# Optimization experiments

Hardware: AMD Instinct MI355X
Metric: run time of the kernel (lower is better)

## Reference

```python
import jax, jax.numpy as jnp
import numpy as np

B, H, S, D = 2, 8, 2048, 64
TEMPERATURE = 8.0  # sqrt(D)
NEG = -1.0e9


def setup_inputs() -> dict:
    key = jax.random.key(0)
    kq, kk, kv, km = jax.random.split(key, 4)
    q = jax.random.normal(kq, (B, H, S, D), dtype=jnp.float32)
    k = jax.random.normal(kk, (B, H, S, D), dtype=jnp.float32)
    v = jax.random.normal(kv, (B, H, S, D), dtype=jnp.float32)
    mask = jax.random.randint(km, (B, 1, 1, S), 0, 2, dtype=jnp.int32)
    return {"q": q, "k": k, "v": v, "mask": mask}


def reference(q, k, v, mask):
    # scores: [B,H,S,S]
    att = jnp.einsum('bhqd,bhkd->bhqk', q / TEMPERATURE, k)
    att = jnp.where(mask == 0, NEG, att)
    att = jax.nn.softmax(att, axis=-1)
    return jnp.einsum('bhqk,bhkd->bhqd', att, v)
```

## Files before the change

kernel.cpp:

```cpp
#include <hip/hip_runtime.h>
#include <hip/hip_bf16.h>

#define SDIM 2048
#define DDIM 64
#define HNUM 8
#define QBLK 64
#define KVBLK 64
#define NTHR 256
#define NT (SDIM / KVBLK)
#define NSPLIT 2
#define LDP 72
#define NEGV -1.0e9f
#define LOG2E 1.44269504088896f
#define FIXMAX 12.0f

#define WS_KH 0u
#define WS_VH 4194304u
#define WS_O1 8388608u
#define WS_ML 12582912u
#define WS_IDX 13107200u
#define WS_CNT 13123584u

typedef __bf16 bf16x8 __attribute__((ext_vector_type(8)));
typedef __bf16 bf16x4 __attribute__((ext_vector_type(4)));
typedef float f32x4 __attribute__((ext_vector_type(4)));
typedef unsigned short u16;
typedef u16 u16x4 __attribute__((ext_vector_type(4)));
typedef u16 u16x8 __attribute__((ext_vector_type(8)));

__device__ __forceinline__ u16 f2bf(float f) {
    unsigned u = __float_as_uint(f);
    u += 0x7FFFu + ((u >> 16) & 1u);
    return (u16)(u >> 16);
}
__device__ __forceinline__ float bf2f(u16 h) {
    return __uint_as_float((unsigned)h << 16);
}

union U8 { u16 u[8]; u16x8 v; bf16x8 b; };

#define GLD16(g, l) __builtin_amdgcn_global_load_lds( \
    (const __attribute__((address_space(1))) unsigned int*)(g), \
    (__attribute__((address_space(3))) unsigned int*)(l), 16, 0, 0)

__global__ __launch_bounds__(NTHR)
void attn_scan(const int* __restrict__ MK, char* __restrict__ ws) {
    const int b = blockIdx.x, t = threadIdx.x;
    const int ln = t & 63, wv = t >> 6;
    const int* m = MK + (size_t)b * SDIM;
    int* idx = (int*)(ws + WS_IDX) + b * SDIM;

    int vals[8], cnt = 0;
    #pragma unroll
    for (int e = 0; e < 8; ++e) {
        vals[e] = m[t * 8 + e];
        cnt += (vals[e] != 0);
    }
    int inc = cnt;
    #pragma unroll
    for (int off = 1; off < 64; off <<= 1) {
        int n = __shfl_up(inc, off);
        if (ln >= off) inc += n;
    }
    __shared__ int wtot[4];
    if (ln == 63) wtot[wv] = inc;
    __syncthreads();
    int wbase = 0;
    #pragma unroll
    for (int w = 0; w < 4; ++w) if (w < wv) wbase += wtot[w];
    const int total = wtot[0] + wtot[1] + wtot[2] + wtot[3];
    int pos = wbase + inc - cnt;
    #pragma unroll
    for (int e = 0; e < 8; ++e)
        if (vals[e]) idx[pos++] = t * 8 + e;
    if (t == 0) ((int*)(ws + WS_CNT))[b] = total;
    #pragma unroll
    for (int e = 0; e < 8; ++e) {
        const int j = t * 8 + e;
        if (j >= total) idx[j] = 0;
    }
}

__global__ __launch_bounds__(NTHR)
void attn_prep(const float* __restrict__ K, const float* __restrict__ V,
               char* __restrict__ ws) {
    __shared__ float sT[64][68];
    const int t = threadIdx.x;
    const int kt = blockIdx.x, bh = blockIdx.y;
    const int kv0 = kt * KVBLK;
    const int cnt = ((const int*)(ws + WS_CNT))[bh >> 3];
    if (kv0 >= ((cnt + KVBLK - 1) & ~(KVBLK - 1))) return;
    const size_t base = (size_t)bh * SDIM * DDIM;
    const int r = t >> 2, c16 = (t & 3) * 16;
    const int sw = (r & 7) << 4;
    const int orig = ((const int*)(ws + WS_IDX))[(bh >> 3) * SDIM + kv0 + r];

    {
        const float* kp = K + base + (size_t)orig * DDIM + c16;
        char* khrow = ws + WS_KH + ((size_t)bh * SDIM + kv0 + r) * 128;
        #pragma unroll
        for (int j = 0; j < 2; ++j) {
            const float4 a = *(const float4*)(kp + 8 * j);
            const float4 c = *(const float4*)(kp + 8 * j + 4);
            float f[8] = {a.x, a.y, a.z, a.w, c.x, c.y, c.z, c.w};
            U8 h;
            #pragma unroll
            for (int e = 0; e < 8; ++e) h.u[e] = f2bf(f[e]);
            *(u16x8*)(khrow + ((2 * c16 + 16 * j) ^ sw)) = h.v;
        }
    }
    {
        const float* vp = V + base + (size_t)orig * DDIM + c16;
        #pragma unroll
        for (int j = 0; j < 4; ++j)
            *(float4*)&sT[r][c16 + 4 * j] = *(const float4*)(vp + 4 * j);
    }
    __syncthreads();
    {
        char* vhrow = ws + WS_VH + ((size_t)(bh * NT + kt) * 64 + r) * 128;
        #pragma unroll
        for (int j2 = 0; j2 < 2; ++j2) {
            U8 h;
            #pragma unroll
            for (int e = 0; e < 8; ++e)
                h.u[e] = f2bf(sT[c16 + 8 * j2 + e][r]);
            *(u16x8*)(vhrow + ((2 * c16 + 16 * j2) ^ sw)) = h.v;
        }
    }
}

__global__ __launch_bounds__(NTHR, 4)
void attn_main(const float* __restrict__ Q, char* __restrict__ ws,
               float* __restrict__ O) {
    __shared__ __align__(16) u16 sK[2][KVBLK * DDIM];
    __shared__ __align__(16) u16 sV[DDIM * KVBLK];
    __shared__ __align__(16) u16 sP[QBLK][LDP];

    const int tid = threadIdx.x;
    const int wv = tid >> 6, ln = tid & 63;
    const int g = ln >> 4, mi = ln & 15;
    const int bh = blockIdx.y, b = bh >> 3;
    const int split = blockIdx.z;
    const size_t base = (size_t)bh * SDIM * DDIM;
    const int qrow = blockIdx.x * QBLK + 16 * wv + mi;

    const int L = ((const int*)(ws + WS_CNT))[b];
    const int nt = (L + KVBLK - 1) >> 6;
    const int half = (nt + 1) >> 1;
    const int t0 = split ? half : 0;
    const int tn = split ? nt : half;

    const int sw = (mi & 7) << 4;
    const int c0 = (16 * g) ^ sw;
    const int c1 = (64 + 16 * g) ^ sw;

    bf16x8 qhi[2], qlo[2];
    {
        const float* qp = Q + base + (size_t)qrow * DDIM;
        #pragma unroll
        for (int ks = 0; ks < 2; ++ks) {
            const float4 a = *(const float4*)(qp + 32 * ks + 8 * g);
            const float4 c = *(const float4*)(qp + 32 * ks + 8 * g + 4);
            float f[8] = {a.x, a.y, a.z, a.w, c.x, c.y, c.z, c.w};
            U8 h, l;
            #pragma unroll
            for (int e = 0; e < 8; ++e) {
                float fs = f[e] * (0.125f * LOG2E);
                u16 hh = f2bf(fs);
                h.u[e] = hh;
                l.u[e] = f2bf(fs - bf2f(hh));
            }
            qhi[ks] = h.b;
            qlo[ks] = l.b;
        }
    }

    const char* kgl = ws + WS_KH + (size_t)bh * SDIM * 128;
    const char* vgl = ws + WS_VH + (size_t)bh * NT * 8192;
    const int chunk = wv * 2;

    f32x4 zero4 = {0.f, 0.f, 0.f, 0.f};
    f32x4 oacc[4];
    #pragma unroll
    for (int i = 0; i < 4; ++i) oacc[i] = zero4;
    float lrun = 0.f;

    if (t0 < tn) {
        {
            const char* src = kgl + (size_t)t0 * 8192;
            #pragma unroll
            for (int p = 0; p < 2; ++p) {
                const int off = (chunk + p) * 1024;
                GLD16(src + off + ln * 16, (char*)&sK[0][0] + off);
            }
        }

        int cur = 0;
        for (int kt = t0; kt < tn; ++kt) {
            {
                const char* src = vgl + (size_t)kt * 8192;
                #pragma unroll
                for (int p = 0; p < 2; ++p) {
                    const int off = (chunk + p) * 1024;
                    GLD16(src + off + ln * 16, (char*)&sV[0] + off);
                }
            }
            {
                const int kn = (kt + 1 < tn) ? kt + 1 : t0;
                const char* src = kgl + (size_t)kn * 8192;
                char* dst = (char*)&sK[cur ^ 1][0];
                #pragma unroll
                for (int p = 0; p < 2; ++p) {
                    const int off = (chunk + p) * 1024;
                    GLD16(src + off + ln * 16, dst + off);
                }
            }
            asm volatile("s_waitcnt vmcnt(4)" ::: "memory");
            __builtin_amdgcn_s_barrier();

            const char* kb = (const char*)&sK[cur][0] + mi * 128;
            float s[4][4];
            #pragma unroll
            for (int mt = 0; mt < 4; ++mt) {
                f32x4 acc = zero4;
                const bf16x8 ah0 = *(const bf16x8*)(kb + mt * 2048 + c0);
                const bf16x8 ah1 = *(const bf16x8*)(kb + mt * 2048 + c1);
                acc = __builtin_amdgcn_mfma_f32_16x16x32_bf16(ah0, qhi[0], acc, 0, 0, 0);
                acc = __builtin_amdgcn_mfma_f32_16x16x32_bf16(ah0, qlo[0], acc, 0, 0, 0);
                acc = __builtin_amdgcn_mfma_f32_16x16x32_bf16(ah1, qhi[1], acc, 0, 0, 0);
                acc = __builtin_amdgcn_mfma_f32_16x16x32_bf16(ah1, qlo[1], acc, 0, 0, 0);
                s[mt][0] = acc[0]; s[mt][1] = acc[1];
                s[mt][2] = acc[2]; s[mt][3] = acc[3];
            }
            const int rem = L - kt * KVBLK;
            if (rem < KVBLK) {
                #pragma unroll
                for (int mt = 0; mt < 4; ++mt)
                    #pragma unroll
                    for (int r = 0; r < 4; ++r)
                        if (16 * mt + 4 * g + r >= rem) s[mt][r] = NEGV;
            }

            #pragma unroll
            for (int mt = 0; mt < 4; ++mt) {
                bf16x4 pw;
                #pragma unroll
                for (int r = 0; r < 4; ++r) {
                    const float p = __builtin_amdgcn_exp2f(s[mt][r] - FIXMAX);
                    pw[r] = (__bf16)p;
                    lrun += p;
                }
                *(bf16x4*)&sP[16 * wv + mi][16 * mt + 4 * g] = pw;
            }

            asm volatile("s_waitcnt vmcnt(2)" ::: "memory");
            __builtin_amdgcn_s_barrier();

            const char* vb = (const char*)&sV[0] + mi * 128;
            const bf16x8 pf0 = *(const bf16x8*)&sP[16 * wv + mi][8 * g];
            const bf16x8 pf1 = *(const bf16x8*)&sP[16 * wv + mi][32 + 8 * g];
            #pragma unroll
            for (int mt = 0; mt < 4; ++mt) {
                const bf16x8 vh0 = *(const bf16x8*)(vb + mt * 2048 + c0);
                const bf16x8 vh1 = *(const bf16x8*)(vb + mt * 2048 + c1);
                oacc[mt] = __builtin_amdgcn_mfma_f32_16x16x32_bf16(vh0, pf0, oacc[mt], 0, 0, 0);
                oacc[mt] = __builtin_amdgcn_mfma_f32_16x16x32_bf16(vh1, pf1, oacc[mt], 0, 0, 0);
            }
            __builtin_amdgcn_s_barrier();
            cur ^= 1;
        }
    }

    lrun += __shfl_xor(lrun, 16);
    lrun += __shfl_xor(lrun, 32);
    const float inv = lrun > 0.f ? 1.0f / lrun : 0.f;
    if (split == 0) {
        float* op = O + base + (size_t)qrow * DDIM;
        #pragma unroll
        for (int mt = 0; mt < 4; ++mt) {
            float4 o;
            o.x = oacc[mt][0] * inv;
            o.y = oacc[mt][1] * inv;
            o.z = oacc[mt][2] * inv;
            o.w = oacc[mt][3] * inv;
            *(float4*)(op + 16 * mt + 4 * g) = o;
        }
    } else {
        u16* op1 = (u16*)(ws + WS_O1) + ((size_t)bh * SDIM + qrow) * DDIM;
        #pragma unroll
        for (int mt = 0; mt < 4; ++mt) {
            u16x4 o;
            #pragma unroll
            for (int r = 0; r < 4; ++r) o[r] = f2bf(oacc[mt][r] * inv);
            *(u16x4*)(op1 + 16 * mt + 4 * g) = o;
        }
    }
    if (g == 0) {
        float* lp = (float*)(ws + WS_ML) + ((size_t)(split * 2 * HNUM + bh) * SDIM + qrow);
        *lp = lrun;
    }
}

__global__ __launch_bounds__(NTHR)
void attn_combine(const char* __restrict__ ws, float* __restrict__ O) {
    const int t = threadIdx.x;
    const size_t grow = (size_t)blockIdx.x * 16 + (t >> 4);
    const int e4 = (t & 15) * 4;
    const float* ml = (const float*)(ws + WS_ML);
    float w0 = ml[grow];
    float w1 = ml[(size_t)2 * HNUM * SDIM + grow];
    const float swt = w0 + w1;
    const float inv = swt > 0.f ? 1.0f / swt : 0.f;
    w0 *= inv; w1 *= inv;
    float* op = O + grow * DDIM + e4;
    const float4 o0 = *(const float4*)op;
    const u16x4 o1 = *(const u16x4*)((const u16*)(ws + WS_O1) + grow * DDIM + e4);
    float4 r;
    r.x = o0.x * w0 + bf2f(o1[0]) * w1;
    r.y = o0.y * w0 + bf2f(o1[1]) * w1;
    r.z = o0.z * w0 + bf2f(o1[2]) * w1;
    r.w = o0.w * w0 + bf2f(o1[3]) * w1;
    *(float4*)op = r;
}

extern "C" void kernel_launch(void* const* d_in, const int* in_sizes, int n_in,
                              void* d_out, int out_size, void* d_ws, size_t ws_size,
                              hipStream_t stream) {
    const float* q  = (const float*)d_in[0];
    const float* k  = (const float*)d_in[1];
    const float* v  = (const float*)d_in[2];
    const int*   mk = (const int*)d_in[3];
    float* o = (float*)d_out;
    char* ws = (char*)d_ws;

    attn_scan<<<2, NTHR, 0, stream>>>(mk, ws);

    dim3 pgrid(NT, 2 * HNUM);
    attn_prep<<<pgrid, NTHR, 0, stream>>>(k, v, ws);

    dim3 grid(SDIM / QBLK, 2 * HNUM, NSPLIT);
    attn_main<<<grid, NTHR, 0, stream>>>(q, ws, o);

    dim3 cgrid((2 * HNUM * SDIM) / 16);
    attn_combine<<<cgrid, NTHR, 0, stream>>>(ws, o);
}
```

Baseline: 41.14 us.

## Split KV across waves with register-held P and cross-wave LDS reduction

Restructures attn_main so each wave handles a 16-key quarter of every KV tile for all 64 query rows, instead of 16 query rows against all keys. P stays in registers and feeds a 16x16x16 bf16 MFMA directly, which removes the sP LDS round trip and the per-tile barriers. The V pre-pack layout changes to suit that. Q is now a single bf16 term instead of the hi/lo split, halving QK MFMAs at some accuracy cost. The partial outputs are summed through LDS at the end. This adds a final reduction and raises register pressure (launch bound 3).

```diff
diff --git a/kernel.cpp b/kernel.cpp
--- a/kernel.cpp
+++ b/kernel.cpp
@@ -9,7 +9,6 @@
 #define NTHR 256
 #define NT (SDIM / KVBLK)
 #define NSPLIT 2
-#define LDP 72
 #define NEGV -1.0e9f
 #define LOG2E 1.44269504088896f
 #define FIXMAX 12.0f
@@ -23,6 +22,7 @@
 
 typedef __bf16 bf16x8 __attribute__((ext_vector_type(8)));
 typedef __bf16 bf16x4 __attribute__((ext_vector_type(4)));
+typedef short s16x4 __attribute__((ext_vector_type(4)));
 typedef float f32x4 __attribute__((ext_vector_type(4)));
 typedef unsigned short u16;
 typedef u16 u16x4 __attribute__((ext_vector_type(4)));
@@ -42,6 +42,15 @@
 #define GLD16(g, l) __builtin_amdgcn_global_load_lds( \
     (const __attribute__((address_space(1))) unsigned int*)(g), \
     (__attribute__((address_space(3))) unsigned int*)(l), 16, 0, 0)
+
+__device__ __forceinline__ f32x4 mfma16(s16x4 a, s16x4 b, f32x4 c) {
+#if __has_builtin(__builtin_amdgcn_mfma_f32_16x16x16bf16_1k)
+    return __builtin_amdgcn_mfma_f32_16x16x16bf16_1k(a, b, c, 0, 0, 0);
+#else
+    asm("v_mfma_f32_16x16x16_bf16 %0, %1, %2, %0" : "+v"(c) : "v"(a), "v"(b));
+    return c;
+#endif
+}
 
 __global__ __launch_bounds__(NTHR)
 void attn_scan(const int* __restrict__ MK, char* __restrict__ ws) {
@@ -117,24 +126,26 @@
     }
     __syncthreads();
     {
-        char* vhrow = ws + WS_VH + ((size_t)(bh * NT + kt) * 64 + r) * 128;
-        #pragma unroll
-        for (int j2 = 0; j2 < 2; ++j2) {
-            U8 h;
-            #pragma unroll
-            for (int e = 0; e < 8; ++e)
-                h.u[e] = f2bf(sT[c16 + 8 * j2 + e][r]);
-            *(u16x8*)(vhrow + ((2 * c16 + 16 * j2) ^ sw)) = h.v;
-        }
-    }
-}
-
-__global__ __launch_bounds__(NTHR, 4)
+        const int kvq = t >> 6, d = t & 63;
+        char* dst = ws + WS_VH + ((size_t)(bh * NT + kt)) * 8192 + kvq * 2048 + d * 32;
+        #pragma unroll
+        for (int gk = 0; gk < 4; ++gk) {
+            u16x4 h;
+            #pragma unroll
+            for (int e = 0; e < 4; ++e)
+                h[e] = f2bf(sT[kvq * 16 + 4 * gk + e][d]);
+            *(u16x4*)(dst + (((gk ^ ((d >> 2) & 3)) << 3))) = h;
+        }
+    }
+}
+
+__global__ __launch_bounds__(NTHR, 3)
 void attn_main(const float* __restrict__ Q, char* __restrict__ ws,
                float* __restrict__ O) {
-    __shared__ __align__(16) u16 sK[2][KVBLK * DDIM];
-    __shared__ __align__(16) u16 sV[DDIM * KVBLK];
-    __shared__ __align__(16) u16 sP[QBLK][LDP];
+    __shared__ __align__(16) union LdsU {
+        struct { u16 k[2][4096]; u16 v[2][4096]; } st;
+        struct { float o[3][64][64]; float l[4][64]; } red;
+    } lds;
 
     const int tid = threadIdx.x;
     const int wv = tid >> 6, ln = tid & 63;
@@ -142,7 +153,7 @@
     const int bh = blockIdx.y, b = bh >> 3;
     const int split = blockIdx.z;
     const size_t base = (size_t)bh * SDIM * DDIM;
-    const int qrow = blockIdx.x * QBLK + 16 * wv + mi;
+    const int q0 = blockIdx.x * QBLK;
 
     const int L = ((const int*)(ws + WS_CNT))[b];
     const int nt = (L + KVBLK - 1) >> 6;
@@ -153,152 +164,152 @@
     const int sw = (mi & 7) << 4;
     const int c0 = (16 * g) ^ sw;
     const int c1 = (64 + 16 * g) ^ sw;
-
-    bf16x8 qhi[2], qlo[2];
-    {
-        const float* qp = Q + base + (size_t)qrow * DDIM;
+    const int vslot = (g ^ (mi >> 2)) << 3;
+
+    bf16x8 qf[4][2];
+    #pragma unroll
+    for (int qt = 0; qt < 4; ++qt) {
+        const float* qp = Q + base + (size_t)(q0 + qt * 16 + mi) * DDIM;
         #pragma unroll
         for (int ks = 0; ks < 2; ++ks) {
             const float4 a = *(const float4*)(qp + 32 * ks + 8 * g);
             const float4 c = *(const float4*)(qp + 32 * ks + 8 * g + 4);
             float f[8] = {a.x, a.y, a.z, a.w, c.x, c.y, c.z, c.w};
-            U8 h, l;
-            #pragma unroll
-            for (int e = 0; e < 8; ++e) {
-                float fs = f[e] * (0.125f * LOG2E);
-                u16 hh = f2bf(fs);
-                h.u[e] = hh;
-                l.u[e] = f2bf(fs - bf2f(hh));
-            }
-            qhi[ks] = h.b;
-            qlo[ks] = l.b;
-        }
-    }
-
-    const char* kgl = ws + WS_KH + (size_t)bh * SDIM * 128;
-    const char* vgl = ws + WS_VH + (size_t)bh * NT * 8192;
-    const int chunk = wv * 2;
+            U8 h;
+            #pragma unroll
+            for (int e = 0; e < 8; ++e) h.u[e] = f2bf(f[e] * (0.125f * LOG2E));
+            qf[qt][ks] = h.b;
+        }
+    }
+
+    const char* kq_src = ws + WS_KH + (size_t)bh * SDIM * 128;
+    const char* vq_src = ws + WS_VH + (size_t)bh * NT * 8192;
+    char* sKbase = (char*)lds.st.k;
+    char* sVbase = (char*)lds.st.v;
 
     f32x4 zero4 = {0.f, 0.f, 0.f, 0.f};
-    f32x4 oacc[4];
-    #pragma unroll
-    for (int i = 0; i < 4; ++i) oacc[i] = zero4;
-    float lrun = 0.f;
+    f32x4 oacc[4][4];
+    #pragma unroll
+    for (int i = 0; i < 4; ++i)
+        #pragma unroll
+        for (int j = 0; j < 4; ++j) oacc[i][j] = zero4;
+    float lrun[4] = {0.f, 0.f, 0.f, 0.f};
+
+#define STAGE_QTR(kt_, buf_) do { \
+    const char* ksrc_ = kq_src + (size_t)(kt_) * 8192 + wv * 2048; \
+    char* kdst_ = sKbase + (buf_) * 8192 + wv * 2048; \
+    GLD16(ksrc_ + ln * 16, kdst_); \
+    GLD16(ksrc_ + 1024 + ln * 16, kdst_ + 1024); \
+    const char* vsrc_ = vq_src + (size_t)(kt_) * 8192 + wv * 2048; \
+    char* vdst_ = sVbase + (buf_) * 8192 + wv * 2048; \
+    GLD16(vsrc_ + ln * 16, vdst_); \
+    GLD16(vsrc_ + 1024 + ln * 16, vdst_ + 1024); \
+} while (0)
 
     if (t0 < tn) {
-        {
-            const char* src = kgl + (size_t)t0 * 8192;
-            #pragma unroll
-            for (int p = 0; p < 2; ++p) {
-                const int off = (chunk + p) * 1024;
-                GLD16(src + off + ln * 16, (char*)&sK[0][0] + off);
-            }
-        }
-
+        STAGE_QTR(t0, 0);
         int cur = 0;
         for (int kt = t0; kt < tn; ++kt) {
-            {
-                const char* src = vgl + (size_t)kt * 8192;
+            const int kn = (kt + 1 < tn) ? kt + 1 : t0;
+            STAGE_QTR(kn, cur ^ 1);
+            asm volatile("s_waitcnt vmcnt(4)" ::: "memory");
+
+            const char* kb = sKbase + cur * 8192 + wv * 2048 + mi * 128;
+            const bf16x8 a0 = *(const bf16x8*)(kb + c0);
+            const bf16x8 a1 = *(const bf16x8*)(kb + c1);
+            f32x4 s[4];
+            #pragma unroll
+            for (int qt = 0; qt < 4; ++qt) {
+                f32x4 acc = zero4;
+                acc = __builtin_amdgcn_mfma_f32_16x16x32_bf16(a0, qf[qt][0], acc, 0, 0, 0);
+                acc = __builtin_amdgcn_mfma_f32_16x16x32_bf16(a1, qf[qt][1], acc, 0, 0, 0);
+                s[qt] = acc;
+            }
+            const int kbase = kt * KVBLK + wv * 16;
+            if (kbase + 16 > L) {
                 #pragma unroll
-                for (int p = 0; p < 2; ++p) {
-                    const int off = (chunk + p) * 1024;
-                    GLD16(src + off + ln * 16, (char*)&sV[0] + off);
-                }
-            }
-            {
-                const int kn = (kt + 1 < tn) ? kt + 1 : t0;
-                const char* src = kgl + (size_t)kn * 8192;
-                char* dst = (char*)&sK[cur ^ 1][0];
-                #pragma unroll
-                for (int p = 0; p < 2; ++p) {
-                    const int off = (chunk + p) * 1024;
-                    GLD16(src + off + ln * 16, dst + off);
-                }
-            }
-            asm volatile("s_waitcnt vmcnt(4)" ::: "memory");
-            __builtin_amdgcn_s_barrier();
-
-            const char* kb = (const char*)&sK[cur][0] + mi * 128;
-            float s[4][4];
-            #pragma unroll
-            for (int mt = 0; mt < 4; ++mt) {
-                f32x4 acc = zero4;
-                const bf16x8 ah0 = *(const bf16x8*)(kb + mt * 2048 + c0);
-                const bf16x8 ah1 = *(const bf16x8*)(kb + mt * 2048 + c1);
-                acc = __builtin_amdgcn_mfma_f32_16x16x32_bf16(ah0, qhi[0], acc, 0, 0, 0);
-                acc = __builtin_amdgcn_mfma_f32_16x16x32_bf16(ah0, qlo[0], acc, 0, 0, 0);
-                acc = __builtin_amdgcn_mfma_f32_16x16x32_bf16(ah1, qhi[1], acc, 0, 0, 0);
-                acc = __builtin_amdgcn_mfma_f32_16x16x32_bf16(ah1, qlo[1], acc, 0, 0, 0);
-                s[mt][0] = acc[0]; s[mt][1] = acc[1];
-                s[mt][2] = acc[2]; s[mt][3] = acc[3];
-            }
-            const int rem = L - kt * KVBLK;
-            if (rem < KVBLK) {
-                #pragma unroll
-                for (int mt = 0; mt < 4; ++mt)
+                for (int qt = 0; qt < 4; ++qt)
                     #pragma unroll
                     for (int r = 0; r < 4; ++r)
-                        if (16 * mt + 4 * g + r >= rem) s[mt][r] = NEGV;
-            }
-
-            #pragma unroll
-            for (int mt = 0; mt < 4; ++mt) {
-                bf16x4 pw;
+                        if (kbase + 4 * g + r >= L) s[qt][r] = NEGV;
+            }
+
+            bf16x4 pw[4];
+            #pragma unroll
+            for (int qt = 0; qt < 4; ++qt) {
                 #pragma unroll
                 for (int r = 0; r < 4; ++r) {
-                    const float p = __builtin_amdgcn_exp2f(s[mt][r] - FIXMAX);
-                    pw[r] = (__bf16)p;
-                    lrun += p;
+                    const float p = __builtin_amdgcn_exp2f(s[qt][r] - FIXMAX);
+                    pw[qt][r] = (__bf16)p;
+                    lrun[qt] += p;
                 }
-                *(bf16x4*)&sP[16 * wv + mi][16 * mt + 4 * g] = pw;
-            }
-
-            asm volatile("s_waitcnt vmcnt(2)" ::: "memory");
-            __builtin_amdgcn_s_barrier();
-
-            const char* vb = (const char*)&sV[0] + mi * 128;
-            const bf16x8 pf0 = *(const bf16x8*)&sP[16 * wv + mi][8 * g];
-            const bf16x8 pf1 = *(const bf16x8*)&sP[16 * wv + mi][32 + 8 * g];
-            #pragma unroll
-            for (int mt = 0; mt < 4; ++mt) {
-                const bf16x8 vh0 = *(const bf16x8*)(vb + mt * 2048 + c0);
-                const bf16x8 vh1 = *(const bf16x8*)(vb + mt * 2048 + c1);
-                oacc[mt] = __builtin_amdgcn_mfma_f32_16x16x32_bf16(vh0, pf0, oacc[mt], 0, 0, 0);
-                oacc[mt] = __builtin_amdgcn_mfma_f32_16x16x32_bf16(vh1, pf1, oacc[mt], 0, 0, 0);
-            }
-            __builtin_amdgcn_s_barrier();
+            }
+
+            const char* vb = sVbase + cur * 8192 + wv * 2048 + mi * 32 + vslot;
+            #pragma unroll
+            for (int dt = 0; dt < 4; ++dt) {
+                const s16x4 vf = *(const s16x4*)(vb + dt * 512);
+                #pragma unroll
+                for (int qt = 0; qt < 4; ++qt)
+                    oacc[qt][dt] = mfma16(vf, __builtin_bit_cast(s16x4, pw[qt]), oacc[qt][dt]);
+            }
             cur ^= 1;
         }
     }
 
-    lrun += __shfl_xor(lrun, 16);
-    lrun += __shfl_xor(lrun, 32);
-    const float inv = lrun > 0.f ? 1.0f / lrun : 0.f;
-    if (split == 0) {
-        float* op = O + base + (size_t)qrow * DDIM;
-        #pragma unroll
-        for (int mt = 0; mt < 4; ++mt) {
-            float4 o;
-            o.x = oacc[mt][0] * inv;
-            o.y = oacc[mt][1] * inv;
-            o.z = oacc[mt][2] * inv;
-            o.w = oacc[mt][3] * inv;
-            *(float4*)(op + 16 * mt + 4 * g) = o;
-        }
-    } else {
-        u16* op1 = (u16*)(ws + WS_O1) + ((size_t)bh * SDIM + qrow) * DDIM;
-        #pragma unroll
-        for (int mt = 0; mt < 4; ++mt) {
-            u16x4 o;
-            #pragma unroll
-            for (int r = 0; r < 4; ++r) o[r] = f2bf(oacc[mt][r] * inv);
-            *(u16x4*)(op1 + 16 * mt + 4 * g) = o;
-        }
+    #pragma unroll
+    for (int qt = 0; qt < 4; ++qt) {
+        lrun[qt] += __shfl_xor(lrun[qt], 16);
+        lrun[qt] += __shfl_xor(lrun[qt], 32);
+    }
+    asm volatile("s_waitcnt vmcnt(0)" ::: "memory");
+    __syncthreads();
+    if (wv > 0) {
+        #pragma unroll
+        for (int qt = 0; qt < 4; ++qt)
+            #pragma unroll
+            for (int dt = 0; dt < 4; ++dt)
+                *(f32x4*)&lds.red.o[wv - 1][qt * 16 + mi][16 * dt + 4 * g] = oacc[qt][dt];
     }
     if (g == 0) {
-        float* lp = (float*)(ws + WS_ML) + ((size_t)(split * 2 * HNUM + bh) * SDIM + qrow);
-        *lp = lrun;
-    }
+        #pragma unroll
+        for (int qt = 0; qt < 4; ++qt)
+            lds.red.l[wv][qt * 16 + mi] = lrun[qt];
+    }
+    __syncthreads();
+    if (wv == 0) {
+        #pragma unroll
+        for (int qt = 0; qt < 4; ++qt) {
+            const int q = qt * 16 + mi;
+            const float l = lds.red.l[0][q] + lds.red.l[1][q] +
+                            lds.red.l[2][q] + lds.red.l[3][q];
+            const float inv = l > 0.f ? 1.0f / l : 0.f;
+            const int qrow = q0 + q;
+            #pragma unroll
+            for (int dt = 0; dt < 4; ++dt) {
+                f32x4 o = oacc[qt][dt];
+                #pragma unroll
+                for (int w = 0; w < 3; ++w)
+                    o += *(const f32x4*)&lds.red.o[w][q][16 * dt + 4 * g];
+                o *= inv;
+                if (split == 0) {
+                    *(f32x4*)(O + base + (size_t)qrow * DDIM + 16 * dt + 4 * g) = o;
+                } else {
+                    u16* op1 = (u16*)(ws + WS_O1) + ((size_t)bh * SDIM + qrow) * DDIM;
+                    u16x4 ob;
+                    #pragma unroll
+                    for (int r = 0; r < 4; ++r) ob[r] = f2bf(o[r]);
+                    *(u16x4*)(op1 + 16 * dt + 4 * g) = ob;
+                }
+            }
+            if (g == 0) {
+                float* lp = (float*)(ws + WS_ML) +
+                            ((size_t)(split * 2 * HNUM + bh) * SDIM + qrow);
+                *lp = l;
+            }
+        }
+    }
+#undef STAGE_QTR
 }
 
 __global__ __launch_bounds__(NTHR)
```

Measured after the change: 49.33 us. 1.2x slower.

## Keep P in registers via 16x16x16 MFMA, drop Q hi/lo split, double-buffer V

Applied to the files above, without the earlier changes.

V is now stored in a layout matched to the 16x16x16 bf16 MFMA B-operand, so the softmax probabilities can be fed straight from registers into the PV product. This removes the shared-memory P staging buffer and the mid-iteration barrier. Q is no longer split into bf16 hi/lo parts, which halves the QK MFMA count at the cost of score precision. K and V are both double-buffered and prefetched together, which adds LDS use and retunes the wait counts.

```diff
diff --git a/kernel.cpp b/kernel.cpp
--- a/kernel.cpp
+++ b/kernel.cpp
@@ -9,7 +9,6 @@
 #define NTHR 256
 #define NT (SDIM / KVBLK)
 #define NSPLIT 2
-#define LDP 72
 #define NEGV -1.0e9f
 #define LOG2E 1.44269504088896f
 #define FIXMAX 12.0f
@@ -23,6 +22,7 @@
 
 typedef __bf16 bf16x8 __attribute__((ext_vector_type(8)));
 typedef __bf16 bf16x4 __attribute__((ext_vector_type(4)));
+typedef short s16x4 __attribute__((ext_vector_type(4)));
 typedef float f32x4 __attribute__((ext_vector_type(4)));
 typedef unsigned short u16;
 typedef u16 u16x4 __attribute__((ext_vector_type(4)));
@@ -42,6 +42,15 @@
 #define GLD16(g, l) __builtin_amdgcn_global_load_lds( \
     (const __attribute__((address_space(1))) unsigned int*)(g), \
     (__attribute__((address_space(3))) unsigned int*)(l), 16, 0, 0)
+
+__device__ __forceinline__ f32x4 mfma16(s16x4 a, s16x4 b, f32x4 c) {
+#if __has_builtin(__builtin_amdgcn_mfma_f32_16x16x16bf16_1k)
+    return __builtin_amdgcn_mfma_f32_16x16x16bf16_1k(a, b, c, 0, 0, 0);
+#else
+    asm("v_mfma_f32_16x16x16_bf16 %0, %1, %2, %0" : "+v"(c) : "v"(a), "v"(b));
+    return c;
+#endif
+}
 
 __global__ __launch_bounds__(NTHR)
 void attn_scan(const int* __restrict__ MK, char* __restrict__ ws) {
@@ -117,14 +126,15 @@
     }
     __syncthreads();
     {
-        char* vhrow = ws + WS_VH + ((size_t)(bh * NT + kt) * 64 + r) * 128;
-        #pragma unroll
-        for (int j2 = 0; j2 < 2; ++j2) {
-            U8 h;
-            #pragma unroll
-            for (int e = 0; e < 8; ++e)
-                h.u[e] = f2bf(sT[c16 + 8 * j2 + e][r]);
-            *(u16x8*)(vhrow + ((2 * c16 + 16 * j2) ^ sw)) = h.v;
+        const int mt = t >> 6, d = t & 63;
+        char* dst = ws + WS_VH + ((size_t)(bh * NT + kt)) * 8192 + mt * 2048 + d * 32;
+        #pragma unroll
+        for (int gk = 0; gk < 4; ++gk) {
+            u16x4 h;
+            #pragma unroll
+            for (int e = 0; e < 4; ++e)
+                h[e] = f2bf(sT[mt * 16 + 4 * gk + e][d]);
+            *(u16x4*)(dst + (((gk ^ ((d >> 2) & 3)) << 3))) = h;
         }
     }
 }
@@ -132,9 +142,8 @@
 __global__ __launch_bounds__(NTHR, 4)
 void attn_main(const float* __restrict__ Q, char* __restrict__ ws,
                float* __restrict__ O) {
-    __shared__ __align__(16) u16 sK[2][KVBLK * DDIM];
-    __shared__ __align__(16) u16 sV[DDIM * KVBLK];
-    __shared__ __align__(16) u16 sP[QBLK][LDP];
+    __shared__ __align__(16) u16 sK[2][4096];
+    __shared__ __align__(16) u16 sV[2][4096];
 
     const int tid = threadIdx.x;
     const int wv = tid >> 6, ln = tid & 63;
@@ -153,8 +162,9 @@
     const int sw = (mi & 7) << 4;
     const int c0 = (16 * g) ^ sw;
     const int c1 = (64 + 16 * g) ^ sw;
-
-    bf16x8 qhi[2], qlo[2];
+    const int vslot = (g ^ (mi >> 2)) << 3;
+
+    bf16x8 qf[2];
     {
         const float* qp = Q + base + (size_t)qrow * DDIM;
         #pragma unroll
@@ -162,75 +172,52 @@
             const float4 a = *(const float4*)(qp + 32 * ks + 8 * g);
             const float4 c = *(const float4*)(qp + 32 * ks + 8 * g + 4);
             float f[8] = {a.x, a.y, a.z, a.w, c.x, c.y, c.z, c.w};
-            U8 h, l;
-            #pragma unroll
-            for (int e = 0; e < 8; ++e) {
-                float fs = f[e] * (0.125f * LOG2E);
-                u16 hh = f2bf(fs);
-                h.u[e] = hh;
-                l.u[e] = f2bf(fs - bf2f(hh));
-            }
-            qhi[ks] = h.b;
-            qlo[ks] = l.b;
+            U8 h;
+            #pragma unroll
+            for (int e = 0; e < 8; ++e) h.u[e] = f2bf(f[e] * (0.125f * LOG2E));
+            qf[ks] = h.b;
         }
     }
 
     const char* kgl = ws + WS_KH + (size_t)bh * SDIM * 128;
     const char* vgl = ws + WS_VH + (size_t)bh * NT * 8192;
-    const int chunk = wv * 2;
 
     f32x4 zero4 = {0.f, 0.f, 0.f, 0.f};
     f32x4 oacc[4];
     #pragma unroll
     for (int i = 0; i < 4; ++i) oacc[i] = zero4;
-    float lrun = 0.f;
+    float lr0 = 0.f, lr1 = 0.f, lr2 = 0.f, lr3 = 0.f;
+
+#define STAGE_T(kt_, buf_) do { \
+    const char* ksrc_ = kgl + (size_t)(kt_) * 8192 + wv * 2048; \
+    char* kdst_ = (char*)&sK[buf_][0] + wv * 2048; \
+    GLD16(ksrc_ + ln * 16, kdst_); \
+    GLD16(ksrc_ + 1024 + ln * 16, kdst_ + 1024); \
+    const char* vsrc_ = vgl + (size_t)(kt_) * 8192 + wv * 2048; \
+    char* vdst_ = (char*)&sV[buf_][0] + wv * 2048; \
+    GLD16(vsrc_ + ln * 16, vdst_); \
+    GLD16(vsrc_ + 1024 + ln * 16, vdst_ + 1024); \
+} while (0)
 
     if (t0 < tn) {
-        {
-            const char* src = kgl + (size_t)t0 * 8192;
-            #pragma unroll
-            for (int p = 0; p < 2; ++p) {
-                const int off = (chunk + p) * 1024;
-                GLD16(src + off + ln * 16, (char*)&sK[0][0] + off);
-            }
-        }
-
+        STAGE_T(t0, 0);
         int cur = 0;
         for (int kt = t0; kt < tn; ++kt) {
-            {
-                const char* src = vgl + (size_t)kt * 8192;
-                #pragma unroll
-                for (int p = 0; p < 2; ++p) {
-                    const int off = (chunk + p) * 1024;
-                    GLD16(src + off + ln * 16, (char*)&sV[0] + off);
-                }
-            }
-            {
-                const int kn = (kt + 1 < tn) ? kt + 1 : t0;
-                const char* src = kgl + (size_t)kn * 8192;
-                char* dst = (char*)&sK[cur ^ 1][0];
-                #pragma unroll
-                for (int p = 0; p < 2; ++p) {
-                    const int off = (chunk + p) * 1024;
-                    GLD16(src + off + ln * 16, dst + off);
-                }
-            }
+            const int kn = (kt + 1 < tn) ? kt + 1 : t0;
+            STAGE_T(kn, cur ^ 1);
             asm volatile("s_waitcnt vmcnt(4)" ::: "memory");
             __builtin_amdgcn_s_barrier();
 
             const char* kb = (const char*)&sK[cur][0] + mi * 128;
-            float s[4][4];
+            f32x4 s[4];
             #pragma unroll
             for (int mt = 0; mt < 4; ++mt) {
                 f32x4 acc = zero4;
-                const bf16x8 ah0 = *(const bf16x8*)(kb + mt * 2048 + c0);
-                const bf16x8 ah1 = *(const bf16x8*)(kb + mt * 2048 + c1);
-                acc = __builtin_amdgcn_mfma_f32_16x16x32_bf16(ah0, qhi[0], acc, 0, 0, 0);
-                acc = __builtin_amdgcn_mfma_f32_16x16x32_bf16(ah0, qlo[0], acc, 0, 0, 0);
-                acc = __builtin_amdgcn_mfma_f32_16x16x32_bf16(ah1, qhi[1], acc, 0, 0, 0);
-                acc = __builtin_amdgcn_mfma_f32_16x16x32_bf16(ah1, qlo[1], acc, 0, 0, 0);
-                s[mt][0] = acc[0]; s[mt][1] = acc[1];
-                s[mt][2] = acc[2]; s[mt][3] = acc[3];
+                const bf16x8 a0 = *(const bf16x8*)(kb + mt * 2048 + c0);
+                const bf16x8 a1 = *(const bf16x8*)(kb + mt * 2048 + c1);
+                acc = __builtin_amdgcn_mfma_f32_16x16x32_bf16(a0, qf[0], acc, 0, 0, 0);
+                acc = __builtin_amdgcn_mfma_f32_16x16x32_bf16(a1, qf[1], acc, 0, 0, 0);
+                s[mt] = acc;
             }
             const int rem = L - kt * KVBLK;
             if (rem < KVBLK) {
@@ -241,58 +228,61 @@
                         if (16 * mt + 4 * g + r >= rem) s[mt][r] = NEGV;
             }
 
+            bf16x4 pw[4];
             #pragma unroll
             for (int mt = 0; mt < 4; ++mt) {
-                bf16x4 pw;
+                float psum = 0.f;
                 #pragma unroll
                 for (int r = 0; r < 4; ++r) {
                     const float p = __builtin_amdgcn_exp2f(s[mt][r] - FIXMAX);
-                    pw[r] = (__bf16)p;
-                    lrun += p;
+                    pw[mt][r] = (__bf16)p;
+                    psum += p;
                 }
-                *(bf16x4*)&sP[16 * wv + mi][16 * mt + 4 * g] = pw;
+                if (mt == 0) lr0 += psum;
+                else if (mt == 1) lr1 += psum;
+                else if (mt == 2) lr2 += psum;
+                else lr3 += psum;
             }
 
-            asm volatile("s_waitcnt vmcnt(2)" ::: "memory");
-            __builtin_amdgcn_s_barrier();
-
-            const char* vb = (const char*)&sV[0] + mi * 128;
-            const bf16x8 pf0 = *(const bf16x8*)&sP[16 * wv + mi][8 * g];
-            const bf16x8 pf1 = *(const bf16x8*)&sP[16 * wv + mi][32 + 8 * g];
-            #pragma unroll
-            for (int mt = 0; mt < 4; ++mt) {
-                const bf16x8 vh0 = *(const bf16x8*)(vb + mt * 2048 + c0);
-                const bf16x8 vh1 = *(const bf16x8*)(vb + mt * 2048 + c1);
-                oacc[mt] = __builtin_amdgcn_mfma_f32_16x16x32_bf16(vh0, pf0, oacc[mt], 0, 0, 0);
-                oacc[mt] = __builtin_amdgcn_mfma_f32_16x16x32_bf16(vh1, pf1, oacc[mt], 0, 0, 0);
+            const char* vb = (const char*)&sV[cur][0] + mi * 32 + vslot;
+            #pragma unroll
+            for (int dt = 0; dt < 4; ++dt) {
+                #pragma unroll
+                for (int mt = 0; mt < 4; ++mt) {
+                    const s16x4 vf = *(const s16x4*)(vb + mt * 2048 + dt * 512);
+                    oacc[dt] = mfma16(vf, __builtin_bit_cast(s16x4, pw[mt]), oacc[dt]);
+                }
             }
             __builtin_amdgcn_s_barrier();
             cur ^= 1;
         }
     }
-
+#undef STAGE_T
+
+    float lrun = lr0 + lr1 + lr2 + lr3;
     lrun += __shfl_xor(lrun, 16);
     lrun += __shfl_xor(lrun, 32);
+    asm volatile("s_waitcnt vmcnt(0)" ::: "memory");
     const float inv = lrun > 0.f ? 1.0f / lrun : 0.f;
     if (split == 0) {
         float* op = O + base + (size_t)qrow * DDIM;
         #pragma unroll
-        for (int mt = 0; mt < 4; ++mt) {
+        for (int dt = 0; dt < 4; ++dt) {
             float4 o;
-            o.x = oacc[mt][0] * inv;
-            o.y = oacc[mt][1] * inv;
-            o.z = oacc[mt][2] * inv;
-            o.w = oacc[mt][3] * inv;
-            *(float4*)(op + 16 * mt + 4 * g) = o;
+            o.x = oacc[dt][0] * inv;
+            o.y = oacc[dt][1] * inv;
+            o.z = oacc[dt][2] * inv;
+            o.w = oacc[dt][3] * inv;
+            *(float4*)(op + 16 * dt + 4 * g) = o;
         }
     } else {
         u16* op1 = (u16*)(ws + WS_O1) + ((size_t)bh * SDIM + qrow) * DDIM;
         #pragma unroll
-        for (int mt = 0; mt < 4; ++mt) {
+        for (int dt = 0; dt < 4; ++dt) {
             u16x4 o;
             #pragma unroll
-            for (int r = 0; r < 4; ++r) o[r] = f2bf(oacc[mt][r] * inv);
-            *(u16x4*)(op1 + 16 * mt + 4 * g) = o;
+            for (int r = 0; r < 4; ++r) o[r] = f2bf(oacc[dt][r] * inv);
+            *(u16x4*)(op1 + 16 * dt + 4 * g) = o;
         }
     }
     if (g == 0) {
```

Result: no change. 40.66 us (-1.2%).
